# Kernel tuning notes

Measured on AMD Instinct MI355X. Metric: run time of the kernel, lower is better.

The kernel has to match this reference:

```python
import jax, jax.numpy as jnp
import numpy as np


def _gru_layer(x, W_ih, W_hh, b_ih, b_hh):
    # x: [B, T, in]; W_ih: [3H, in]; W_hh: [3H, H]; gate order (r, z, n) as in PyTorch.
    B, T, _ = x.shape
    H = W_hh.shape[1]
    # Precompute input-side gate pre-activations for the whole sequence (batched GEMM).
    gi = jnp.einsum('bti,gi->btg', x, W_ih) + b_ih  # [B, T, 3H]

    def step(h, gi_t):
        gh = h @ W_hh.T + b_hh                      # [B, 3H]
        i_r, i_z, i_n = jnp.split(gi_t, 3, axis=-1)
        h_r, h_z, h_n = jnp.split(gh, 3, axis=-1)
        r = jax.nn.sigmoid(i_r + h_r)
        z = jax.nn.sigmoid(i_z + h_z)
        n = jnp.tanh(i_n + r * h_n)
        h_new = (1.0 - z) * n + z * h
        return h_new, h_new

    h0 = jnp.zeros((B, H), x.dtype)
    _, hs = jax.lax.scan(step, h0, jnp.swapaxes(gi, 0, 1))  # hs: [T, B, H]
    return jnp.swapaxes(hs, 0, 1)                            # [B, T, H]


def setup_inputs() -> dict:
    key = jax.random.key(0)
    ks = jax.random.split(key, 11)
    B, T, I, H, O = 512, 512, 64, 128, 1
    s = 0.1  # keep gate pre-activations out of saturation
    return {
        'x':     jax.random.normal(ks[0], (B, T, I), jnp.float32),
        'W_ih0': jax.random.normal(ks[1], (3 * H, I), jnp.float32) * s,
        'W_hh0': jax.random.normal(ks[2], (3 * H, H), jnp.float32) * s,
        'b_ih0': jax.random.normal(ks[3], (3 * H,), jnp.float32) * s,
        'b_hh0': jax.random.normal(ks[4], (3 * H,), jnp.float32) * s,
        'W_ih1': jax.random.normal(ks[5], (3 * H, H), jnp.float32) * s,
        'W_hh1': jax.random.normal(ks[6], (3 * H, H), jnp.float32) * s,
        'b_ih1': jax.random.normal(ks[7], (3 * H,), jnp.float32) * s,
        'b_hh1': jax.random.normal(ks[8], (3 * H,), jnp.float32) * s,
        'W_fc':  jax.random.normal(ks[9], (O, H), jnp.float32) * s,
        'b_fc':  jax.random.normal(ks[10], (O,), jnp.float32) * s,
    }


def reference(x, W_ih0, W_hh0, b_ih0, b_hh0, W_ih1, W_hh1, b_ih1, b_hh1, W_fc, b_fc):
    h1 = _gru_layer(x, W_ih0, W_hh0, b_ih0, b_hh0)   # [B, T, H]
    h2 = _gru_layer(h1, W_ih1, W_hh1, b_ih1, b_hh1)  # [B, T, H]
    return h2[:, -1, :] @ W_fc.T + b_fc               # [B, O]
```

## Files before the change

### kernel.cpp

```cpp
#include <hip/hip_runtime.h>
#include <stdint.h>

typedef __bf16 bf16x8 __attribute__((ext_vector_type(8)));
typedef float  floatx4 __attribute__((ext_vector_type(4)));
typedef int    i32x4  __attribute__((ext_vector_type(4)));

#define T_LEN 512
#define BT    4
#define NTHR  512
#define XS    72
#define HIS   144
#define HFS   132

#if __has_builtin(__builtin_amdgcn_exp2f)
#define EXP2(x) __builtin_amdgcn_exp2f(x)
#else
#define EXP2(x) exp2f(x)
#endif

#define MFMA_BF(a,b,c)  __builtin_amdgcn_mfma_f32_16x16x32_bf16((a),(b),(c),0,0,0)
#define MFMA_I8(a,b,c)  __builtin_amdgcn_mfma_i32_16x16x64_i8((a),(b),(c),0,0,0)

#define L2E   1.4426950408889634f
#define S_RZ  (-L2E / (254.f * 127.f))
#define S_N   (-2.f * L2E / (254.f * 127.f))

__device__ __forceinline__ float rcpf(float x) { return __builtin_amdgcn_rcpf(x); }

__device__ __forceinline__ bf16x8 wfrag_bf(const float* W, int ldk, int row, int k0, float scale) {
    const float* p = W + (size_t)row * ldk + k0;
    bf16x8 r;
    #pragma unroll
    for (int j = 0; j < 8; ++j) r[j] = (__bf16)(p[j] * scale);
    return r;
}
__device__ __forceinline__ i32x4 wfrag_i8(const float* W, int ldk, int row, int k0) {
    const float* p = W + (size_t)row * ldk + k0;
    i32x4 r;
    #pragma unroll
    for (int d = 0; d < 4; ++d) {
        uint32_t dw = 0;
        #pragma unroll
        for (int j = 0; j < 4; ++j) {
            float q = __builtin_rintf(p[d * 4 + j] * 254.f);
            q = fminf(127.f, fmaxf(-127.f, q));
            dw |= ((uint32_t)((int)q & 0xff)) << (8 * j);
        }
        r[d] = (int)dw;
    }
    return r;
}

__global__ __launch_bounds__(NTHR, 2) void gru_fused(
    const float* __restrict__ x,
    const float* __restrict__ Wih0, const float* __restrict__ Whh0,
    const float* __restrict__ bih0, const float* __restrict__ bhh0,
    const float* __restrict__ Wih1, const float* __restrict__ Whh1,
    const float* __restrict__ bih1, const float* __restrict__ bhh1,
    const float* __restrict__ Wfc,  const float* __restrict__ bfc,
    float* __restrict__ out)
{
    __shared__ __align__(16) __bf16      xb[2][16 * XS];
    __shared__ __align__(16) signed char h0i[2][16 * HIS];
    __shared__ __align__(16) signed char h1i[2][16 * HIS];
    __shared__ __align__(16) float       hfin[16 * HFS];

    const int tid  = threadIdx.x;
    const int lane = tid & 63;
    const int ln16 = lane & 15;
    const int quad = lane >> 4;
    const int q8   = quad * 8;
    const int q16  = quad * 16;
    const int wave = tid >> 6;
    const int wv   = wave & 3;
    const int brow = blockIdx.x * BT;

    for (int i = tid; i < 16 * HIS; i += NTHR) {
        h0i[0][i] = 0; h0i[1][i] = 0;
        h1i[0][i] = 0; h1i[1][i] = 0;
    }
    for (int i = tid; i < 16 * XS; i += NTHR) {
        xb[0][i] = (__bf16)0.f; xb[1][i] = (__bf16)0.f;
    }

    float hf[2] = {0.f, 0.f};

    if (wave < 4) {
        float bRZ[2], bNi[2], bNh[2];
        bf16x8 wI[2][3][2];
        i32x4  wH[2][3][2];
        #pragma unroll
        for (int t2 = 0; t2 < 2; ++t2) {
            const int c = wv * 32 + t2 * 16 + ln16;
            bRZ[t2] = 0.f;
            bNi[t2] = -2.f * L2E * bih0[256 + c];
            bNh[t2] = -2.f * L2E * bhh0[256 + c];
            #pragma unroll
            for (int g = 0; g < 3; ++g) {
                const int row = g * 128 + c;
                const float sc = (g == 2) ? (-2.f * L2E) : (-L2E);
                #pragma unroll
                for (int q = 0; q < 2; ++q) {
                    wI[t2][g][q] = wfrag_bf(Wih0, 64, row, q * 32 + q8, sc);
                    wH[t2][g][q] = wfrag_i8(Whh0, 128, row, q * 64 + q16);
                }
            }
        }
        float bR[2], bZ[2];
        #pragma unroll
        for (int t2 = 0; t2 < 2; ++t2) {
            const int c = wv * 32 + t2 * 16 + ln16;
            bR[t2] = -L2E * (bih0[c] + bhh0[c]);
            bZ[t2] = -L2E * (bih0[128 + c] + bhh0[128 + c]);
        }

        const int sb = tid >> 6, sc = tid & 63;
        const float* xp = x + (size_t)(brow + sb) * T_LEN * 64 + sc;
        float vx0 = xp[0];
        float vx1 = xp[64];

        for (int tt = 0; tt <= T_LEN; ++tt) {
            xb[tt & 1][(sb * 4) * XS + sc] = (__bf16)vx0;
            __syncthreads();
            vx0 = vx1;
            {
                const int tnext = (tt + 2 < T_LEN) ? tt + 2 : T_LEN - 1;
                vx1 = xp[(size_t)tnext * 64];
            }

            if (tt < T_LEN) {
                const int R = tt & 1, Wn = R ^ 1;
                bf16x8 ax0 = *(const bf16x8*)&xb[R][ln16 * XS + q8];
                bf16x8 ax1 = *(const bf16x8*)&xb[R][ln16 * XS + 32 + q8];
                i32x4 ah[2];
                #pragma unroll
                for (int q = 0; q < 2; ++q)
                    ah[q] = *(const i32x4*)&h0i[R][ln16 * HIS + q * 64 + q16];

                #pragma unroll
                for (int t2 = 0; t2 < 2; ++t2) {
                    floatx4 fR  = {bR[t2],  bR[t2],  bR[t2],  bR[t2]};
                    floatx4 fZ  = {bZ[t2],  bZ[t2],  bZ[t2],  bZ[t2]};
                    floatx4 fNi = {bNi[t2], bNi[t2], bNi[t2], bNi[t2]};
                    i32x4 cR = {0,0,0,0}, cZ = {0,0,0,0}, cNh = {0,0,0,0};
                    fR  = MFMA_BF(ax0, wI[t2][0][0], fR);  fR  = MFMA_BF(ax1, wI[t2][0][1], fR);
                    fZ  = MFMA_BF(ax0, wI[t2][1][0], fZ);  fZ  = MFMA_BF(ax1, wI[t2][1][1], fZ);
                    fNi = MFMA_BF(ax0, wI[t2][2][0], fNi); fNi = MFMA_BF(ax1, wI[t2][2][1], fNi);
                    #pragma unroll
                    for (int q = 0; q < 2; ++q) {
                        cR  = MFMA_I8(ah[q], wH[t2][0][q], cR);
                        cZ  = MFMA_I8(ah[q], wH[t2][1][q], cZ);
                        cNh = MFMA_I8(ah[q], wH[t2][2][q], cNh);
                    }
                    const float pr  = fmaf((float)cR[0],  S_RZ, fR[0]);
                    const float pz  = fmaf((float)cZ[0],  S_RZ, fZ[0]);
                    const float phn = fmaf((float)cNh[0], S_N,  bNh[t2]);
                    const float r = rcpf(1.f + EXP2(pr));
                    const float z = rcpf(1.f + EXP2(pz));
                    const float n = 2.f * rcpf(1.f + EXP2(fmaf(r, phn, fNi[0]))) - 1.f;
                    const float h = n + z * (hf[t2] - n);
                    hf[t2] = h;
                    const int cc = wv * 32 + t2 * 16 + ln16;
                    h0i[Wn][(quad * 4) * HIS + cc] =
                        (signed char)(int)__builtin_rintf(h * 127.f);
                }
            }
        }
    } else {
        float bRZ1[2], bNi1[2], bNh1[2];
        i32x4 wI[2][3][2], wH[2][3][2];
        #pragma unroll
        for (int t2 = 0; t2 < 2; ++t2) {
            const int c = wv * 32 + t2 * 16 + ln16;
            bRZ1[t2] = 0.f;
            bNi1[t2] = -2.f * L2E * bih1[256 + c];
            bNh1[t2] = -2.f * L2E * bhh1[256 + c];
            #pragma unroll
            for (int g = 0; g < 3; ++g) {
                const int row = g * 128 + c;
                #pragma unroll
                for (int q = 0; q < 2; ++q) {
                    wI[t2][g][q] = wfrag_i8(Wih1, 128, row, q * 64 + q16);
                    wH[t2][g][q] = wfrag_i8(Whh1, 128, row, q * 64 + q16);
                }
            }
        }
        float bR1[2], bZ1[2];
        #pragma unroll
        for (int t2 = 0; t2 < 2; ++t2) {
            const int c = wv * 32 + t2 * 16 + ln16;
            bR1[t2] = -L2E * (bih1[c] + bhh1[c]);
            bZ1[t2] = -L2E * (bih1[128 + c] + bhh1[128 + c]);
        }

        for (int tt = 0; tt <= T_LEN; ++tt) {
            __syncthreads();
            if (tt > 0) {
                const int R = tt & 1, Wn = R ^ 1;
                i32x4 ah[2], a1[2];
                #pragma unroll
                for (int q = 0; q < 2; ++q) {
                    ah[q] = *(const i32x4*)&h0i[R][ln16 * HIS + q * 64 + q16];
                    a1[q] = *(const i32x4*)&h1i[R][ln16 * HIS + q * 64 + q16];
                }
                #pragma unroll
                for (int t2 = 0; t2 < 2; ++t2) {
                    i32x4 cR = {0,0,0,0}, cZ = {0,0,0,0};
                    i32x4 cNi = {0,0,0,0}, cNh = {0,0,0,0};
                    #pragma unroll
                    for (int q = 0; q < 2; ++q) {
                        cR  = MFMA_I8(ah[q], wI[t2][0][q], cR);
                        cZ  = MFMA_I8(ah[q], wI[t2][1][q], cZ);
                        cNi = MFMA_I8(ah[q], wI[t2][2][q], cNi);
                    }
                    #pragma unroll
                    for (int q = 0; q < 2; ++q) {
                        cR  = MFMA_I8(a1[q], wH[t2][0][q], cR);
                        cZ  = MFMA_I8(a1[q], wH[t2][1][q], cZ);
                        cNh = MFMA_I8(a1[q], wH[t2][2][q], cNh);
                    }
                    const float pr  = fmaf((float)cR[0],  S_RZ, bR1[t2]);
                    const float pz  = fmaf((float)cZ[0],  S_RZ, bZ1[t2]);
                    const float pin = fmaf((float)cNi[0], S_N,  bNi1[t2]);
                    const float phn = fmaf((float)cNh[0], S_N,  bNh1[t2]);
                    const float r = rcpf(1.f + EXP2(pr));
                    const float z = rcpf(1.f + EXP2(pz));
                    const float n = 2.f * rcpf(1.f + EXP2(fmaf(r, phn, pin))) - 1.f;
                    const float h = n + z * (hf[t2] - n);
                    hf[t2] = h;
                    const int cc = wv * 32 + t2 * 16 + ln16;
                    h1i[Wn][(quad * 4) * HIS + cc] =
                        (signed char)(int)__builtin_rintf(h * 127.f);
                }
            }
        }
        #pragma unroll
        for (int t2 = 0; t2 < 2; ++t2)
            hfin[(quad * 4) * HFS + wv * 32 + t2 * 16 + ln16] = hf[t2];
    }

    __syncthreads();
    {
        const int row = tid >> 5, l = tid & 31;
        if ((row & 3) == 0) {
            float s = 0.f;
            #pragma unroll
            for (int k = 0; k < 4; ++k)
                s += hfin[row * HFS + l + 32 * k] * Wfc[l + 32 * k];
            #pragma unroll
            for (int d = 16; d >= 1; d >>= 1) s += __shfl_down(s, d, 32);
            if (l == 0) out[brow + (row >> 2)] = s + bfc[0];
        }
    }
}

extern "C" void kernel_launch(void* const* d_in, const int* in_sizes, int n_in,
                              void* d_out, int out_size, void* d_ws, size_t ws_size,
                              hipStream_t stream) {
    const float* x    = (const float*)d_in[0];
    const float* Wih0 = (const float*)d_in[1];
    const float* Whh0 = (const float*)d_in[2];
    const float* bih0 = (const float*)d_in[3];
    const float* bhh0 = (const float*)d_in[4];
    const float* Wih1 = (const float*)d_in[5];
    const float* Whh1 = (const float*)d_in[6];
    const float* bih1 = (const float*)d_in[7];
    const float* bhh1 = (const float*)d_in[8];
    const float* Wfc  = (const float*)d_in[9];
    const float* bfc  = (const float*)d_in[10];
    float* out = (float*)d_out;

    hipLaunchKernelGGL(gru_fused, dim3(512 / BT), dim3(NTHR), 0, stream,
                       x, Wih0, Whh0, bih0, bhh0, Wih1, Whh1, bih1, bhh1, Wfc, bfc, out);
}
```

Baseline: 419.1 us.

## Software-pipeline input-side GRU matmuls off the recurrent critical path

Layer 0 now computes the input-projection MFMAs for step t+1 after finishing step t's recurrence, so each step's critical path holds only the hidden-state MFMAs and gate math. Layer 1 likewise precomputes its h0-driven input contributions one step ahead and seeds the recurrent accumulators with them. The pipeline depth grows by one step, and the x prefetch distance and buffer indexing are adjusted to match. This costs extra registers for the carried partial sums and a subtler double-buffer schedule.

```diff
diff --git a/kernel.cpp b/kernel.cpp
--- a/kernel.cpp
+++ b/kernel.cpp
@@ -82,19 +82,21 @@
     for (int i = tid; i < 16 * XS; i += NTHR) {
         xb[0][i] = (__bf16)0.f; xb[1][i] = (__bf16)0.f;
     }
+    __syncthreads();
 
     float hf[2] = {0.f, 0.f};
 
     if (wave < 4) {
-        float bRZ[2], bNi[2], bNh[2];
+        float bNi[2], bNh[2], bR[2], bZ[2];
         bf16x8 wI[2][3][2];
         i32x4  wH[2][3][2];
         #pragma unroll
         for (int t2 = 0; t2 < 2; ++t2) {
             const int c = wv * 32 + t2 * 16 + ln16;
-            bRZ[t2] = 0.f;
             bNi[t2] = -2.f * L2E * bih0[256 + c];
             bNh[t2] = -2.f * L2E * bhh0[256 + c];
+            bR[t2]  = -L2E * (bih0[c] + bhh0[c]);
+            bZ[t2]  = -L2E * (bih0[128 + c] + bhh0[128 + c]);
             #pragma unroll
             for (int g = 0; g < 3; ++g) {
                 const int row = g * 128 + c;
@@ -106,75 +108,94 @@
                 }
             }
         }
-        float bR[2], bZ[2];
-        #pragma unroll
-        for (int t2 = 0; t2 < 2; ++t2) {
-            const int c = wv * 32 + t2 * 16 + ln16;
-            bR[t2] = -L2E * (bih0[c] + bhh0[c]);
-            bZ[t2] = -L2E * (bih0[128 + c] + bhh0[128 + c]);
-        }
-
-        const int sb = tid >> 6, sc = tid & 63;
-        const float* xp = x + (size_t)(brow + sb) * T_LEN * 64 + sc;
-        float vx0 = xp[0];
-        float vx1 = xp[64];
-
-        for (int tt = 0; tt <= T_LEN; ++tt) {
-            xb[tt & 1][(sb * 4) * XS + sc] = (__bf16)vx0;
+
+        const int sb = tid >> 6, scg = tid & 63;
+        const float* xp = x + (size_t)(brow + sb) * T_LEN * 64 + scg;
+        xb[0][(sb * 4) * XS + scg] = (__bf16)xp[0];
+        xb[1][(sb * 4) * XS + scg] = (__bf16)xp[64];
+        float vx = xp[2 * 64];
+        __syncthreads();
+
+        floatx4 pF[2][3];
+        {
+            bf16x8 ax0 = *(const bf16x8*)&xb[0][ln16 * XS + q8];
+            bf16x8 ax1 = *(const bf16x8*)&xb[0][ln16 * XS + 32 + q8];
+            #pragma unroll
+            for (int t2 = 0; t2 < 2; ++t2) {
+                floatx4 fR  = {bR[t2],  bR[t2],  bR[t2],  bR[t2]};
+                floatx4 fZ  = {bZ[t2],  bZ[t2],  bZ[t2],  bZ[t2]};
+                floatx4 fNi = {bNi[t2], bNi[t2], bNi[t2], bNi[t2]};
+                fR  = MFMA_BF(ax0, wI[t2][0][0], fR);  fR  = MFMA_BF(ax1, wI[t2][0][1], fR);
+                fZ  = MFMA_BF(ax0, wI[t2][1][0], fZ);  fZ  = MFMA_BF(ax1, wI[t2][1][1], fZ);
+                fNi = MFMA_BF(ax0, wI[t2][2][0], fNi); fNi = MFMA_BF(ax1, wI[t2][2][1], fNi);
+                pF[t2][0] = fR; pF[t2][1] = fZ; pF[t2][2] = fNi;
+            }
+        }
+
+        for (int tt = 0; tt <= T_LEN + 1; ++tt) {
+            __builtin_amdgcn_sched_barrier(0);
             __syncthreads();
-            vx0 = vx1;
+            xb[tt & 1][(sb * 4) * XS + scg] = (__bf16)vx;
             {
-                const int tnext = (tt + 2 < T_LEN) ? tt + 2 : T_LEN - 1;
-                vx1 = xp[(size_t)tnext * 64];
+                int tl = tt + 3; if (tl > T_LEN - 1) tl = T_LEN - 1;
+                vx = xp[(size_t)tl * 64];
             }
 
             if (tt < T_LEN) {
-                const int R = tt & 1, Wn = R ^ 1;
-                bf16x8 ax0 = *(const bf16x8*)&xb[R][ln16 * XS + q8];
-                bf16x8 ax1 = *(const bf16x8*)&xb[R][ln16 * XS + 32 + q8];
+                const int Rp = (tt + 1) & 1, Wc = tt & 1;
                 i32x4 ah[2];
                 #pragma unroll
                 for (int q = 0; q < 2; ++q)
-                    ah[q] = *(const i32x4*)&h0i[R][ln16 * HIS + q * 64 + q16];
-
+                    ah[q] = *(const i32x4*)&h0i[Rp][ln16 * HIS + q * 64 + q16];
                 #pragma unroll
                 for (int t2 = 0; t2 < 2; ++t2) {
-                    floatx4 fR  = {bR[t2],  bR[t2],  bR[t2],  bR[t2]};
-                    floatx4 fZ  = {bZ[t2],  bZ[t2],  bZ[t2],  bZ[t2]};
-                    floatx4 fNi = {bNi[t2], bNi[t2], bNi[t2], bNi[t2]};
                     i32x4 cR = {0,0,0,0}, cZ = {0,0,0,0}, cNh = {0,0,0,0};
-                    fR  = MFMA_BF(ax0, wI[t2][0][0], fR);  fR  = MFMA_BF(ax1, wI[t2][0][1], fR);
-                    fZ  = MFMA_BF(ax0, wI[t2][1][0], fZ);  fZ  = MFMA_BF(ax1, wI[t2][1][1], fZ);
-                    fNi = MFMA_BF(ax0, wI[t2][2][0], fNi); fNi = MFMA_BF(ax1, wI[t2][2][1], fNi);
                     #pragma unroll
                     for (int q = 0; q < 2; ++q) {
                         cR  = MFMA_I8(ah[q], wH[t2][0][q], cR);
                         cZ  = MFMA_I8(ah[q], wH[t2][1][q], cZ);
                         cNh = MFMA_I8(ah[q], wH[t2][2][q], cNh);
                     }
-                    const float pr  = fmaf((float)cR[0],  S_RZ, fR[0]);
-                    const float pz  = fmaf((float)cZ[0],  S_RZ, fZ[0]);
+                    const float pr  = fmaf((float)cR[0],  S_RZ, pF[t2][0][0]);
+                    const float pz  = fmaf((float)cZ[0],  S_RZ, pF[t2][1][0]);
                     const float phn = fmaf((float)cNh[0], S_N,  bNh[t2]);
                     const float r = rcpf(1.f + EXP2(pr));
                     const float z = rcpf(1.f + EXP2(pz));
-                    const float n = 2.f * rcpf(1.f + EXP2(fmaf(r, phn, fNi[0]))) - 1.f;
+                    const float n = 2.f * rcpf(1.f + EXP2(fmaf(r, phn, pF[t2][2][0]))) - 1.f;
                     const float h = n + z * (hf[t2] - n);
                     hf[t2] = h;
                     const int cc = wv * 32 + t2 * 16 + ln16;
-                    h0i[Wn][(quad * 4) * HIS + cc] =
+                    h0i[Wc][(quad * 4) * HIS + cc] =
                         (signed char)(int)__builtin_rintf(h * 127.f);
                 }
             }
+
+            if (tt + 1 < T_LEN) {
+                const int Rn = (tt + 1) & 1;
+                bf16x8 ax0 = *(const bf16x8*)&xb[Rn][ln16 * XS + q8];
+                bf16x8 ax1 = *(const bf16x8*)&xb[Rn][ln16 * XS + 32 + q8];
+                #pragma unroll
+                for (int t2 = 0; t2 < 2; ++t2) {
+                    floatx4 fR  = {bR[t2],  bR[t2],  bR[t2],  bR[t2]};
+                    floatx4 fZ  = {bZ[t2],  bZ[t2],  bZ[t2],  bZ[t2]};
+                    floatx4 fNi = {bNi[t2], bNi[t2], bNi[t2], bNi[t2]};
+                    fR  = MFMA_BF(ax0, wI[t2][0][0], fR);  fR  = MFMA_BF(ax1, wI[t2][0][1], fR);
+                    fZ  = MFMA_BF(ax0, wI[t2][1][0], fZ);  fZ  = MFMA_BF(ax1, wI[t2][1][1], fZ);
+                    fNi = MFMA_BF(ax0, wI[t2][2][0], fNi); fNi = MFMA_BF(ax1, wI[t2][2][1], fNi);
+                    pF[t2][0] = fR; pF[t2][1] = fZ; pF[t2][2] = fNi;
+                }
+            }
         }
     } else {
-        float bRZ1[2], bNi1[2], bNh1[2];
+        float bNi1[2], bNh1[2], bR1[2], bZ1[2];
         i32x4 wI[2][3][2], wH[2][3][2];
         #pragma unroll
         for (int t2 = 0; t2 < 2; ++t2) {
             const int c = wv * 32 + t2 * 16 + ln16;
-            bRZ1[t2] = 0.f;
             bNi1[t2] = -2.f * L2E * bih1[256 + c];
             bNh1[t2] = -2.f * L2E * bhh1[256 + c];
+            bR1[t2]  = -L2E * (bih1[c] + bhh1[c]);
+            bZ1[t2]  = -L2E * (bih1[128 + c] + bhh1[128 + c]);
             #pragma unroll
             for (int g = 0; g < 3; ++g) {
                 const int row = g * 128 + c;
@@ -185,52 +206,58 @@
                 }
             }
         }
-        float bR1[2], bZ1[2];
-        #pragma unroll
-        for (int t2 = 0; t2 < 2; ++t2) {
-            const int c = wv * 32 + t2 * 16 + ln16;
-            bR1[t2] = -L2E * (bih1[c] + bhh1[c]);
-            bZ1[t2] = -L2E * (bih1[128 + c] + bhh1[128 + c]);
-        }
-
-        for (int tt = 0; tt <= T_LEN; ++tt) {
+        __syncthreads();
+
+        i32x4 pI[2][3];
+        for (int tt = 0; tt <= T_LEN + 1; ++tt) {
+            __builtin_amdgcn_sched_barrier(0);
             __syncthreads();
-            if (tt > 0) {
-                const int R = tt & 1, Wn = R ^ 1;
-                i32x4 ah[2], a1[2];
-                #pragma unroll
-                for (int q = 0; q < 2; ++q) {
-                    ah[q] = *(const i32x4*)&h0i[R][ln16 * HIS + q * 64 + q16];
-                    a1[q] = *(const i32x4*)&h1i[R][ln16 * HIS + q * 64 + q16];
-                }
+            if (tt >= 2) {
+                const int Rp = (tt + 1) & 1;
+                const int Wc = tt & 1;
+                i32x4 a1[2];
+                #pragma unroll
+                for (int q = 0; q < 2; ++q)
+                    a1[q] = *(const i32x4*)&h1i[Rp][ln16 * HIS + q * 64 + q16];
                 #pragma unroll
                 for (int t2 = 0; t2 < 2; ++t2) {
-                    i32x4 cR = {0,0,0,0}, cZ = {0,0,0,0};
-                    i32x4 cNi = {0,0,0,0}, cNh = {0,0,0,0};
+                    i32x4 cR = pI[t2][0], cZ = pI[t2][1], cNh = {0,0,0,0};
+                    #pragma unroll
+                    for (int q = 0; q < 2; ++q) {
+                        cR  = MFMA_I8(a1[q], wH[t2][0][q], cR);
+                        cZ  = MFMA_I8(a1[q], wH[t2][1][q], cZ);
+                        cNh = MFMA_I8(a1[q], wH[t2][2][q], cNh);
+                    }
+                    const float pr  = fmaf((float)cR[0],       S_RZ, bR1[t2]);
+                    const float pz  = fmaf((float)cZ[0],       S_RZ, bZ1[t2]);
+                    const float pin = fmaf((float)pI[t2][2][0], S_N, bNi1[t2]);
+                    const float phn = fmaf((float)cNh[0],      S_N,  bNh1[t2]);
+                    const float r = rcpf(1.f + EXP2(pr));
+                    const float z = rcpf(1.f + EXP2(pz));
+                    const float n = 2.f * rcpf(1.f + EXP2(fmaf(r, phn, pin))) - 1.f;
+                    const float h = n + z * (hf[t2] - n);
+                    hf[t2] = h;
+                    const int cc = wv * 32 + t2 * 16 + ln16;
+                    h1i[Wc][(quad * 4) * HIS + cc] =
+                        (signed char)(int)__builtin_rintf(h * 127.f);
+                }
+            }
+            if (tt >= 1 && tt <= T_LEN) {
+                const int Rh = (tt + 1) & 1;
+                i32x4 ah[2];
+                #pragma unroll
+                for (int q = 0; q < 2; ++q)
+                    ah[q] = *(const i32x4*)&h0i[Rh][ln16 * HIS + q * 64 + q16];
+                #pragma unroll
+                for (int t2 = 0; t2 < 2; ++t2) {
+                    i32x4 cR = {0,0,0,0}, cZ = {0,0,0,0}, cNi = {0,0,0,0};
                     #pragma unroll
                     for (int q = 0; q < 2; ++q) {
                         cR  = MFMA_I8(ah[q], wI[t2][0][q], cR);
                         cZ  = MFMA_I8(ah[q], wI[t2][1][q], cZ);
                         cNi = MFMA_I8(ah[q], wI[t2][2][q], cNi);
                     }
-                    #pragma unroll
-                    for (int q = 0; q < 2; ++q) {
-                        cR  = MFMA_I8(a1[q], wH[t2][0][q], cR);
-                        cZ  = MFMA_I8(a1[q], wH[t2][1][q], cZ);
-                        cNh = MFMA_I8(a1[q], wH[t2][2][q], cNh);
-                    }
-                    const float pr  = fmaf((float)cR[0],  S_RZ, bR1[t2]);
-                    const float pz  = fmaf((float)cZ[0],  S_RZ, bZ1[t2]);
-                    const float pin = fmaf((float)cNi[0], S_N,  bNi1[t2]);
-                    const float phn = fmaf((float)cNh[0], S_N,  bNh1[t2]);
-                    const float r = rcpf(1.f + EXP2(pr));
-                    const float z = rcpf(1.f + EXP2(pz));
-                    const float n = 2.f * rcpf(1.f + EXP2(fmaf(r, phn, pin))) - 1.f;
-                    const float h = n + z * (hf[t2] - n);
-                    hf[t2] = h;
-                    const int cc = wv * 32 + t2 * 16 + ln16;
-                    h1i[Wn][(quad * 4) * HIS + cc] =
-                        (signed char)(int)__builtin_rintf(h * 127.f);
+                    pI[t2][0] = cR; pI[t2][1] = cZ; pI[t2][2] = cNi;
                 }
             }
         }
```

Result: slower. 436.3 us (+4.1%).
